# Kernel tuning notes

Hardware: AMD Instinct MI355X
Metric: run time of the kernel (lower is better)

## Reference

```python
import jax, jax.numpy as jnp
import numpy as np

H, W = 32, 32
C = 512
HEADS = 8
HEAD_DIM = C // HEADS
B = 8
GROUPS = 32
EPS = 1e-6
N = H * W


def _rel_indices():
    # (N, N) lookup indices into the (2H-1)*(2W-1) relative-position table
    y = np.arange(H)
    x = np.arange(W)
    y1, x1, y2, x2 = np.meshgrid(y, x, y, x, indexing='ij')
    idx = (y1 - y2 + H - 1) * (2 * W - 1) + (x1 - x2 + W - 1)
    return jnp.asarray(idx.reshape(N, N), dtype=jnp.int32)

REL_IDX = _rel_indices()


def setup_inputs() -> dict:
    key = jax.random.key(0)
    ks = jax.random.split(key, 8)
    s = 0.02
    return {
        'x': jax.random.normal(ks[0], (B, C, H, W), jnp.float32),
        '_1': jnp.zeros((1,), jnp.int32),
        '_2': jnp.zeros((1,), jnp.int32),
        'gamma': jnp.ones((C,), jnp.float32),
        'beta': jnp.zeros((C,), jnp.float32),
        'wq': jax.random.normal(ks[1], (C, C), jnp.float32) * s,
        'bq': jnp.zeros((C,), jnp.float32),
        'wk': jax.random.normal(ks[2], (C, C), jnp.float32) * s,
        'bk': jnp.zeros((C,), jnp.float32),
        'wv': jax.random.normal(ks[3], (C, C), jnp.float32) * s,
        'bv': jnp.zeros((C,), jnp.float32),
        'wproj': jax.random.normal(ks[4], (C, C), jnp.float32) * s,
        'bproj': jnp.zeros((C,), jnp.float32),
        'pos_enc': jax.random.normal(ks[5], (HEADS, (2 * H - 1) * (2 * W - 1)), jnp.float32) * s,
    }


def _group_norm(x, gamma, beta):
    b, c, h, w = x.shape
    xg = x.reshape(b, GROUPS, c // GROUPS, h, w)
    mean = xg.mean(axis=(2, 3, 4), keepdims=True)
    var = xg.var(axis=(2, 3, 4), keepdims=True)
    xg = (xg - mean) * jax.lax.rsqrt(var + EPS)
    x = xg.reshape(b, c, h, w)
    return x * gamma[None, :, None, None] + beta[None, :, None, None]


def reference(x, _1, _2, gamma, beta, wq, bq, wk, bk, wv, bv, wproj, bproj, pos_enc):
    x0 = x
    xn = _group_norm(x, gamma, beta)
    xt = xn.reshape(B, C, N)  # (B, C, N)

    def proj(w, bias):
        # 1x1 conv == channel matmul: (B, C_out, N)
        y = jnp.einsum('oc,bcn->bon', w, xt) + bias[None, :, None]
        # split heads: channel index = head*HEAD_DIM + d -> (B, heads, N, d)
        return y.reshape(B, HEADS, HEAD_DIM, N).transpose(0, 1, 3, 2)

    q = proj(wq, bq)
    k = proj(wk, bk)
    v = proj(wv, bv)

    scale = 1.0 / jnp.sqrt(jnp.float32(HEAD_DIM))
    attn = jnp.einsum('bhqd,bhkd->bhqk', q, k) * scale  # (B, heads, N, N)
    rel_bias = pos_enc[:, REL_IDX]  # (heads, N, N)
    attn = attn + rel_bias[None]
    attn = jax.nn.softmax(attn, axis=-1)

    out = jnp.einsum('bhqk,bhkd->bhqd', attn, v)  # (B, heads, N, d)
    out = out.transpose(0, 1, 3, 2).reshape(B, C, H, W)
    out = jnp.einsum('oc,bchw->bohw', wproj, out) + bproj[None, :, None, None]
    return out + x0
```

## Files before the change

### kernel.cpp

```cpp
#include <hip/hip_runtime.h>
#include <hip/hip_bf16.h>
#include <math.h>

typedef __bf16 bf16_t;
typedef __bf16 bf16x8 __attribute__((ext_vector_type(8)));
typedef __bf16 bf16x4 __attribute__((ext_vector_type(4)));
typedef float  f32x4  __attribute__((ext_vector_type(4)));

#define MFMA16(a, b, c) __builtin_amdgcn_mfma_f32_16x16x32_bf16((a), (b), (c), 0, 0, 0)
#define GLDS16(g, s) __builtin_amdgcn_global_load_lds( \
    (const __attribute__((address_space(1))) void*)(g), \
    (__attribute__((address_space(3))) void*)(s), 16, 0, 0)

#define LOG2E 1.4426950408889634f

__global__ __launch_bounds__(256) void cast_weights(
    const float* __restrict__ wq, const float* __restrict__ wk,
    const float* __restrict__ wv, const float* __restrict__ wp,
    bf16_t* __restrict__ Wqkv, bf16_t* __restrict__ Wp)
{
    const int i = (blockIdx.x * 256 + threadIdx.x) * 4;
#pragma unroll
    for (int j = 0; j < 4; ++j) {
        Wqkv[i + j]          = (bf16_t)wq[i + j];
        Wqkv[262144 + i + j] = (bf16_t)wk[i + j];
        Wqkv[524288 + i + j] = (bf16_t)wv[i + j];
        Wp[i + j]            = (bf16_t)wp[i + j];
    }
}

__global__ __launch_bounds__(256) void bias_kernel(
    const float* __restrict__ pos, bf16_t* __restrict__ Bias2)
{
    const int h   = blockIdx.x >> 6;
    const int qt  = blockIdx.x & 63;
    const int qy  = qt >> 1;
    const int qxb = (qt & 1) * 16;
    const int t = threadIdx.x;
    __shared__ bf16_t ps[32][64];

    for (int i = t; i < 32 * 63; i += 256) {
        const int r = i / 63, dx = i - r * 63;
        ps[r][dx] = (bf16_t)(pos[h * 3969 + (qy + r) * 63 + dx] * LOG2E);
    }
    __syncthreads();

    bf16_t* outb = Bias2 + (((size_t)h * 64 + qt) * 64) * 256;
#pragma unroll
    for (int it = 0; it < 16; ++it) {
        const int idx = t + it * 256;
        const int kt = idx >> 6, l = idx & 63;
        const int qx  = qxb + (l & 15);
        const int nk0 = kt * 16 + (l >> 4) * 4;
        const int ky = nk0 >> 5;
        const int kx0 = nk0 & 31;
        const int r = 31 - ky;
        const int dx0 = qx - kx0 + 31;
        bf16x4 o;
#pragma unroll
        for (int j = 0; j < 4; ++j) o[j] = ps[r][dx0 - j];
        *(bf16x4*)(outb + (size_t)idx * 4) = o;
    }
}

__global__ __launch_bounds__(512) void gn_kernel(
    const float* __restrict__ x, const float* __restrict__ gamma,
    const float* __restrict__ beta, bf16_t* __restrict__ xnT)
{
    const int blk = blockIdx.x;
    const int b = blk >> 5, g = blk & 31;
    const int t = threadIdx.x;
    const int hi = t >> 8, tl = t & 255;
    __shared__ float red[16];
    const float* base = x + ((size_t)b * 512 + g * 16) * 1024;

    f32x4 v[8];
    float s = 0.f, s2 = 0.f;
#pragma unroll
    for (int it = 0; it < 8; ++it) {
        v[it] = *(const f32x4*)(base + (size_t)hi * 8192 + it * 1024 + tl * 4);
#pragma unroll
        for (int j = 0; j < 4; ++j) { s += v[it][j]; s2 += v[it][j] * v[it][j]; }
    }
#pragma unroll
    for (int m = 1; m < 64; m <<= 1) { s += __shfl_xor(s, m); s2 += __shfl_xor(s2, m); }
    const int w = t >> 6;
    if ((t & 63) == 0) { red[w] = s; red[8 + w] = s2; }
    __syncthreads();
    s = 0.f; s2 = 0.f;
#pragma unroll
    for (int i = 0; i < 8; ++i) { s += red[i]; s2 += red[8 + i]; }
    const float mean = s * (1.f / 16384.f);
    const float var  = fmaxf(s2 * (1.f / 16384.f) - mean * mean, 0.f);
    const float rstd = rsqrtf(var + 1e-6f);

    float ga[8], be[8];
#pragma unroll
    for (int it = 0; it < 8; ++it) {
        const int gc = g * 16 + hi * 8 + it;
        ga[it] = gamma[gc] * rstd;
        be[it] = beta[gc] - mean * ga[it];
    }
#pragma unroll
    for (int j = 0; j < 4; ++j) {
        bf16x8 o;
#pragma unroll
        for (int it = 0; it < 8; ++it)
            o[it] = (bf16_t)(v[it][j] * ga[it] + be[it]);
        *(bf16x8*)(xnT + ((size_t)b * 1024 + tl * 4 + j) * 512 + g * 16 + hi * 8) = o;
    }
}

__global__ __launch_bounds__(256) void gemm_bt(
    const bf16_t* __restrict__ A, const bf16_t* __restrict__ Bt, int mode,
    int mtiles,
    const float* __restrict__ bias0, const float* __restrict__ bias1,
    const float* __restrict__ bias2,
    const float* __restrict__ x0, float* __restrict__ outF,
    bf16_t* __restrict__ Qb, bf16_t* __restrict__ Kb, bf16_t* __restrict__ Vb)
{
    const int K  = 512;
    const int g  = blockIdx.x;
    const int xcd = g & 7;
    const int i_  = g >> 3;
    const int m_idx = i_ % mtiles;
    const int n_idx = xcd * 8 + i_ / mtiles;
    const int m0 = m_idx * 128;
    const int n0 = n_idx * 128;
    const int t = threadIdx.x;
    const int l = t & 63, w = t >> 6;
    const int wr = w >> 1, wc = w & 1;
    const int lrow = l & 15, lgrp = l >> 4;

    __shared__ __align__(16) char smem_raw[128 * 136 * 2];
    bf16_t* AsF = (bf16_t*)smem_raw;
    bf16_t* BsF = AsF + 8192;
    bf16_t* Ct  = (bf16_t*)smem_raw;

    f32x4 acc[4][4];
#pragma unroll
    for (int i = 0; i < 4; ++i)
#pragma unroll
        for (int j = 0; j < 4; ++j) acc[i][j] = (f32x4){0.f, 0.f, 0.f, 0.f};

    const bf16_t* gA0 = A  + (size_t)(m0 + w * 16 + (l >> 2)) * K + (l & 3) * 8;
    const bf16_t* gA1 = gA0 + (size_t)64 * K;
    const bf16_t* gB0 = Bt + (size_t)(n0 + w * 16 + (l >> 2)) * K + (l & 3) * 8;
    const bf16_t* gB1 = gB0 + (size_t)64 * K;

    GLDS16(gA0, &AsF[w * 512]);
    GLDS16(gA1, &AsF[2048 + w * 512]);
    GLDS16(gB0, &BsF[w * 512]);
    GLDS16(gB1, &BsF[2048 + w * 512]);
    __syncthreads();

    int cur = 0;
    for (int tk = 0; tk < 16; ++tk) {
        if (tk < 15) {
            const int k0 = (tk + 1) * 32;
            const int nb = cur ^ 1;
            GLDS16(gA0 + k0, &AsF[nb * 4096 + w * 512]);
            GLDS16(gA1 + k0, &AsF[nb * 4096 + 2048 + w * 512]);
            GLDS16(gB0 + k0, &BsF[nb * 4096 + w * 512]);
            GLDS16(gB1 + k0, &BsF[nb * 4096 + 2048 + w * 512]);
        }
        const bf16_t* Asb = AsF + cur * 4096;
        const bf16_t* Bsb = BsF + cur * 4096;
        bf16x8 af[4], bfr[4];
#pragma unroll
        for (int ms = 0; ms < 4; ++ms)
            af[ms] = *(const bf16x8*)&Asb[(wr * 64 + ms * 16 + lrow) * 32 + lgrp * 8];
#pragma unroll
        for (int ns = 0; ns < 4; ++ns)
            bfr[ns] = *(const bf16x8*)&Bsb[(wc * 64 + ns * 16 + lrow) * 32 + lgrp * 8];
#pragma unroll
        for (int ms = 0; ms < 4; ++ms)
#pragma unroll
            for (int ns = 0; ns < 4; ++ns)
                acc[ms][ns] = MFMA16(af[ms], bfr[ns], acc[ms][ns]);
        if (tk < 15) __syncthreads();
        cur ^= 1;
    }

    if (mode == 0) {
        const int which = m0 >> 9;
        const int mq = (m0 >> 7) & 3;
        const float* bias = (which == 0) ? bias0 : (which == 1) ? bias1 : bias2;
        const float scl = (which == 0) ? 0.125f * LOG2E : 1.0f;
        const int b   = n_idx >> 3;
        const int nn0 = (n_idx & 7) * 128;

        __syncthreads();
        if (which < 2) {
            bf16_t* Qk = (which == 0) ? Qb : Kb;
#pragma unroll
            for (int ms = 0; ms < 4; ++ms) {
                const int ml = wr * 64 + ms * 16 + lgrp * 4;
#pragma unroll
                for (int ns = 0; ns < 4; ++ns) {
                    const int nl = wc * 64 + ns * 16 + lrow;
                    bf16x4 pk;
#pragma unroll
                    for (int j = 0; j < 4; ++j)
                        pk[j] = (bf16_t)((acc[ms][ns][j] + bias[mq * 128 + ml + j]) * scl);
                    *(bf16x4*)&Ct[nl * 136 + ml] = pk;
                }
            }
            __syncthreads();
#pragma unroll
            for (int it = 0; it < 8; ++it) {
                const int idx = it * 256 + t;
                const int token = idx >> 4, oc = idx & 15;
                const bf16x8 vv8 = *(const bf16x8*)&Ct[token * 136 + oc * 8];
                const int head = mq * 2 + (oc >> 3);
                const int d = (oc & 7) * 8;
                *(bf16x8*)(Qk + (((size_t)b * 8 + head) * 1024 + nn0 + token) * 64 + d) = vv8;
            }
        } else {
#pragma unroll
            for (int ms = 0; ms < 4; ++ms) {
                const int ml = wr * 64 + ms * 16 + lgrp * 4;
#pragma unroll
                for (int ns = 0; ns < 4; ++ns) {
                    const int nl = wc * 64 + ns * 16 + lrow;
#pragma unroll
                    for (int j = 0; j < 4; ++j)
                        Ct[(ml + j) * 136 + nl] =
                            (bf16_t)(acc[ms][ns][j] + bias[mq * 128 + ml + j]);
                }
            }
            __syncthreads();
#pragma unroll
            for (int it = 0; it < 8; ++it) {
                const int idx = it * 256 + t;
                const int o = idx >> 4, nc = idx & 15;
                const bf16x8 vv8 = *(const bf16x8*)&Ct[o * 136 + nc * 8];
                const int head = mq * 2 + (o >> 6);
                const int d = o & 63;
                *(bf16x8*)(Vb + (((size_t)b * 8 + head) * 64 + d) * 1024 + nn0 + nc * 8) = vv8;
            }
        }
    } else {
#pragma unroll
        for (int ms = 0; ms < 4; ++ms) {
#pragma unroll
            for (int ns = 0; ns < 4; ++ns) {
                const int c  = m0 + wr * 64 + ms * 16 + lgrp * 4;
                const int np = n0 + wc * 64 + ns * 16 + lrow;
                const int b = np >> 10, n = np & 1023;
#pragma unroll
                for (int j = 0; j < 4; ++j) {
                    const size_t idx = ((size_t)b * 512 + c + j) * 1024 + n;
                    outF[idx] = acc[ms][ns][j] + bias0[c + j] + x0[idx];
                }
            }
        }
    }
}

__global__ __launch_bounds__(512) void attn_kernel(
    const bf16_t* __restrict__ Qb, const bf16_t* __restrict__ Kb,
    const bf16_t* __restrict__ Vb, const bf16_t* __restrict__ Bias2,
    bf16_t* __restrict__ Xo)
{
    const int bh = blockIdx.x;
    const int h  = bh & 7;
    const int q0 = blockIdx.y * 128;
    const int t = threadIdx.x;
    const int w = t >> 6, l = t & 63;
    const int lrow = l & 15, lgrp = l >> 4;

    __shared__ __align__(16) bf16_t Ks[128][72];
    __shared__ __align__(16) bf16_t Vs[64][136];
    __shared__ __align__(16) bf16_t Ps[8][16][72];

    const int qrow = q0 + w * 16 + lrow;
    const bf16_t* qbase = Qb + ((size_t)bh * 1024 + qrow) * 64;
    const bf16x8 qf0 = *(const bf16x8*)(qbase + lgrp * 8);
    const bf16x8 qf1 = *(const bf16x8*)(qbase + 32 + lgrp * 8);

    const bf16_t* bb = Bias2 + (((size_t)h * 64 + (q0 >> 4) + w) * 64) * 256;

    bf16x8 ones;
#pragma unroll
    for (int i = 0; i < 8; ++i) ones[i] = (bf16_t)1.0f;

    f32x4 oacc[4], tsacc = (f32x4){0.f, 0.f, 0.f, 0.f};
#pragma unroll
    for (int j = 0; j < 4; ++j) oacc[j] = (f32x4){0.f, 0.f, 0.f, 0.f};

    const int sr2 = t >> 3;
    const int sc2 = (t & 7) * 8;
    const bf16_t* Kg = Kb + ((size_t)bh * 1024 + sr2) * 64 + sc2;
    const bf16_t* Vg = Vb + ((size_t)bh * 64 + sr2) * 1024 + sc2;

    bf16x8 kv0 = *(const bf16x8*)(Kg);
    bf16x8 kv1 = *(const bf16x8*)(Kg + (size_t)64 * 64);
    bf16x8 vv0 = *(const bf16x8*)(Vg);
    bf16x8 vv1 = *(const bf16x8*)(Vg + 64);
    bf16x4 bA[8], bB[8];
#pragma unroll
    for (int k = 0; k < 8; ++k)
        bA[k] = *(const bf16x4*)(bb + (size_t)(k * 64 + l) * 4);

    auto dtile = [&](int it, bf16x4 (&bcur)[8], bf16x4 (&bnxt)[8]) {
        const int nk0 = it * 128;
        __syncthreads();
        *(bf16x8*)&Ks[sr2][sc2]      = kv0;
        *(bf16x8*)&Ks[64 + sr2][sc2] = kv1;
        *(bf16x8*)&Vs[sr2][sc2]      = vv0;
        *(bf16x8*)&Vs[sr2][64 + sc2] = vv1;
        __syncthreads();
        if (it < 7) {
            const int nkn = nk0 + 128;
#pragma unroll
            for (int k = 0; k < 8; ++k)
                bnxt[k] = *(const bf16x4*)(bb + (size_t)((((nkn >> 4)) + k) * 64 + l) * 4);
            kv0 = *(const bf16x8*)(Kg + (size_t)nkn * 64);
            kv1 = *(const bf16x8*)(Kg + (size_t)(nkn + 64) * 64);
            vv0 = *(const bf16x8*)(Vg + nkn);
            vv1 = *(const bf16x8*)(Vg + nkn + 64);
        }

#pragma unroll
        for (int st = 0; st < 2; ++st) {
            f32x4 s[4];
#pragma unroll
            for (int ns = 0; ns < 4; ++ns) {
                const bf16x4 bc = bcur[st * 4 + ns];
                f32x4 z = (f32x4){(float)bc[0], (float)bc[1],
                                  (float)bc[2], (float)bc[3]};
                const bf16x8 kf0 = *(const bf16x8*)&Ks[st * 64 + ns * 16 + lrow][lgrp * 8];
                const bf16x8 kf1 = *(const bf16x8*)&Ks[st * 64 + ns * 16 + lrow][32 + lgrp * 8];
                z = MFMA16(kf0, qf0, z);
                z = MFMA16(kf1, qf1, z);
                s[ns] = z;
            }
#pragma unroll
            for (int ns = 0; ns < 4; ++ns) {
                bf16x4 pk;
                pk[0] = (bf16_t)exp2f(s[ns][0]);
                pk[1] = (bf16_t)exp2f(s[ns][1]);
                pk[2] = (bf16_t)exp2f(s[ns][2]);
                pk[3] = (bf16_t)exp2f(s[ns][3]);
                *(bf16x4*)&Ps[w][lrow][ns * 16 + lgrp * 4] = pk;
            }
            const bf16x8 pf0 = *(const bf16x8*)&Ps[w][lrow][lgrp * 8];
            const bf16x8 pf1 = *(const bf16x8*)&Ps[w][lrow][32 + lgrp * 8];
            tsacc = MFMA16(ones, pf0, tsacc);
            tsacc = MFMA16(ones, pf1, tsacc);
#pragma unroll
            for (int ds = 0; ds < 4; ++ds) {
                const bf16x8 vf0 = *(const bf16x8*)&Vs[ds * 16 + lrow][st * 64 + lgrp * 8];
                const bf16x8 vf1 = *(const bf16x8*)&Vs[ds * 16 + lrow][st * 64 + 32 + lgrp * 8];
                oacc[ds] = MFMA16(vf0, pf0, oacc[ds]);
                oacc[ds] = MFMA16(vf1, pf1, oacc[ds]);
            }
        }
    };

    for (int it2 = 0; it2 < 8; it2 += 2) {
        dtile(it2,     bA, bB);
        dtile(it2 + 1, bB, bA);
    }

    const float inv = 1.0f / tsacc[0];

    const int b = bh >> 3;
    const int q = q0 + w * 16 + lrow;
    bf16_t* xrow = Xo + ((size_t)b * 1024 + q) * 512 + h * 64;
#pragma unroll
    for (int ds = 0; ds < 4; ++ds) {
        bf16x4 o4;
#pragma unroll
        for (int j = 0; j < 4; ++j) o4[j] = (bf16_t)(oacc[ds][j] * inv);
        *(bf16x4*)(xrow + ds * 16 + lgrp * 4) = o4;
    }
}

extern "C" void kernel_launch(void* const* d_in, const int* in_sizes, int n_in,
                              void* d_out, int out_size, void* d_ws, size_t ws_size,
                              hipStream_t stream)
{
    const float* x     = (const float*)d_in[0];
    const float* gamma = (const float*)d_in[3];
    const float* beta  = (const float*)d_in[4];
    const float* wq    = (const float*)d_in[5];
    const float* bq    = (const float*)d_in[6];
    const float* wk    = (const float*)d_in[7];
    const float* bk    = (const float*)d_in[8];
    const float* wv    = (const float*)d_in[9];
    const float* bv    = (const float*)d_in[10];
    const float* wp    = (const float*)d_in[11];
    const float* bp    = (const float*)d_in[12];
    const float* pos   = (const float*)d_in[13];
    float* out = (float*)d_out;

    size_t off = 0;
    char* wsb = (char*)d_ws;
    auto alloc = [&](size_t bytes) { char* p = wsb + off; off += bytes; return p; };
    bf16_t* Wqkv  = (bf16_t*)alloc((size_t)1536 * 512 * 2);
    bf16_t* Wp    = (bf16_t*)alloc((size_t)512 * 512 * 2);
    bf16_t* xnT   = (bf16_t*)alloc((size_t)8192 * 512 * 2);
    bf16_t* Qb    = (bf16_t*)alloc((size_t)8192 * 512 * 2);
    bf16_t* Kb    = (bf16_t*)alloc((size_t)8192 * 512 * 2);
    bf16_t* Vb    = (bf16_t*)alloc((size_t)8192 * 512 * 2);
    bf16_t* Xo    = (bf16_t*)alloc((size_t)8192 * 512 * 2);
    bf16_t* Bias2 = (bf16_t*)alloc((size_t)8 * 64 * 64 * 64 * 4 * 2);

    hipLaunchKernelGGL(cast_weights, dim3(256), dim3(256), 0, stream,
                       wq, wk, wv, wp, Wqkv, Wp);
    hipLaunchKernelGGL(bias_kernel, dim3(512), dim3(256), 0, stream, pos, Bias2);
    hipLaunchKernelGGL(gn_kernel, dim3(256), dim3(512), 0, stream,
                       x, gamma, beta, xnT);
    hipLaunchKernelGGL(gemm_bt, dim3(768), dim3(256), 0, stream,
                       Wqkv, xnT, 0, 12, bq, bk, bv,
                       nullptr, nullptr, Qb, Kb, Vb);
    hipLaunchKernelGGL(attn_kernel, dim3(64, 8), dim3(512), 0, stream,
                       Qb, Kb, Vb, Bias2, Xo);
    hipLaunchKernelGGL(gemm_bt, dim3(256), dim3(256), 0, stream,
                       Wp, Xo, 1, 4, bp, nullptr, nullptr,
                       x, out, nullptr, nullptr, nullptr);
}
```

Before: 97.27 us.

## Triple-buffer GEMM LDS loads with vmcnt waits and raise MFMA wave priority

The GEMM main loop moves from a double-buffered LDS pipeline with __syncthreads to a three-stage ring. Loads run two tiles ahead, ordered by explicit s_waitcnt vmcnt counts and one raw s_barrier per iteration, and the loop is fully unrolled. The aim is to hide global-to-LDS latency and drop one barrier per step. s_setprio brackets around the MFMA blocks in both the GEMM and the attention kernels try to favour waves issuing matrix ops. The cost is more LDS (48KB) and so possibly fewer resident blocks, plus reliance on hand-counted vmcnt values.

```diff
diff --git a/kernel.cpp b/kernel.cpp
--- a/kernel.cpp
+++ b/kernel.cpp
@@ -132,10 +132,8 @@
     const int wr = w >> 1, wc = w & 1;
     const int lrow = l & 15, lgrp = l >> 4;
 
-    __shared__ __align__(16) char smem_raw[128 * 136 * 2];
-    bf16_t* AsF = (bf16_t*)smem_raw;
-    bf16_t* BsF = AsF + 8192;
-    bf16_t* Ct  = (bf16_t*)smem_raw;
+    __shared__ __align__(16) char smem_raw[49152];
+    bf16_t* Ct = (bf16_t*)smem_raw;
 
     f32x4 acc[4][4];
 #pragma unroll
@@ -148,24 +146,26 @@
     const bf16_t* gB0 = Bt + (size_t)(n0 + w * 16 + (l >> 2)) * K + (l & 3) * 8;
     const bf16_t* gB1 = gB0 + (size_t)64 * K;
 
-    GLDS16(gA0, &AsF[w * 512]);
-    GLDS16(gA1, &AsF[2048 + w * 512]);
-    GLDS16(gB0, &BsF[w * 512]);
-    GLDS16(gB1, &BsF[2048 + w * 512]);
-    __syncthreads();
-
-    int cur = 0;
+#define STAGE(s, k0) do {                                                   \
+    bf16_t* As_ = (bf16_t*)(smem_raw + (s) * 16384);                        \
+    bf16_t* Bs_ = (bf16_t*)(smem_raw + (s) * 16384 + 8192);                 \
+    GLDS16(gA0 + (k0), As_ + w * 512);                                      \
+    GLDS16(gA1 + (k0), As_ + 2048 + w * 512);                               \
+    GLDS16(gB0 + (k0), Bs_ + w * 512);                                      \
+    GLDS16(gB1 + (k0), Bs_ + 2048 + w * 512); } while (0)
+
+    STAGE(0, 0);
+    STAGE(1, 32);
+
+#pragma unroll
     for (int tk = 0; tk < 16; ++tk) {
-        if (tk < 15) {
-            const int k0 = (tk + 1) * 32;
-            const int nb = cur ^ 1;
-            GLDS16(gA0 + k0, &AsF[nb * 4096 + w * 512]);
-            GLDS16(gA1 + k0, &AsF[nb * 4096 + 2048 + w * 512]);
-            GLDS16(gB0 + k0, &BsF[nb * 4096 + w * 512]);
-            GLDS16(gB1 + k0, &BsF[nb * 4096 + 2048 + w * 512]);
-        }
-        const bf16_t* Asb = AsF + cur * 4096;
-        const bf16_t* Bsb = BsF + cur * 4096;
+        if (tk < 15) asm volatile("s_waitcnt vmcnt(4)" ::: "memory");
+        else         asm volatile("s_waitcnt vmcnt(0)" ::: "memory");
+        __builtin_amdgcn_s_barrier();
+        __builtin_amdgcn_sched_barrier(0);
+        if (tk + 2 < 16) STAGE((tk + 2) % 3, (tk + 2) * 32);
+        const bf16_t* Asb = (const bf16_t*)(smem_raw + (tk % 3) * 16384);
+        const bf16_t* Bsb = Asb + 4096;
         bf16x8 af[4], bfr[4];
 #pragma unroll
         for (int ms = 0; ms < 4; ++ms)
@@ -173,14 +173,15 @@
 #pragma unroll
         for (int ns = 0; ns < 4; ++ns)
             bfr[ns] = *(const bf16x8*)&Bsb[(wc * 64 + ns * 16 + lrow) * 32 + lgrp * 8];
+        __builtin_amdgcn_s_setprio(1);
 #pragma unroll
         for (int ms = 0; ms < 4; ++ms)
 #pragma unroll
             for (int ns = 0; ns < 4; ++ns)
                 acc[ms][ns] = MFMA16(af[ms], bfr[ns], acc[ms][ns]);
-        if (tk < 15) __syncthreads();
-        cur ^= 1;
-    }
+        __builtin_amdgcn_s_setprio(0);
+    }
+#undef STAGE
 
     if (mode == 0) {
         const int which = m0 >> 9;
@@ -332,8 +333,10 @@
                                   (float)bc[2], (float)bc[3]};
                 const bf16x8 kf0 = *(const bf16x8*)&Ks[st * 64 + ns * 16 + lrow][lgrp * 8];
                 const bf16x8 kf1 = *(const bf16x8*)&Ks[st * 64 + ns * 16 + lrow][32 + lgrp * 8];
+                __builtin_amdgcn_s_setprio(1);
                 z = MFMA16(kf0, qf0, z);
                 z = MFMA16(kf1, qf1, z);
+                __builtin_amdgcn_s_setprio(0);
                 s[ns] = z;
             }
 #pragma unroll
@@ -347,6 +350,7 @@
             }
             const bf16x8 pf0 = *(const bf16x8*)&Ps[w][lrow][lgrp * 8];
             const bf16x8 pf1 = *(const bf16x8*)&Ps[w][lrow][32 + lgrp * 8];
+            __builtin_amdgcn_s_setprio(1);
             tsacc = MFMA16(ones, pf0, tsacc);
             tsacc = MFMA16(ones, pf1, tsacc);
 #pragma unroll
@@ -356,6 +360,7 @@
                 oacc[ds] = MFMA16(vf0, pf0, oacc[ds]);
                 oacc[ds] = MFMA16(vf1, pf1, oacc[ds]);
             }
+            __builtin_amdgcn_s_setprio(0);
         }
     };
 
```

Result: slower. 102.9 us (+5.7%).
